# Kernel tuning notes

Hardware: AMD Instinct MI355X
Metric: run time of the kernel (lower is better)

## Reference

```python
import jax, jax.numpy as jnp
import numpy as np

D_MODEL = 1024
N_HEADS = 16
HEAD_DIM = D_MODEL // N_HEADS
LENGTHS = np.array([1536, 1024, 1400, 900, 1200, 1300, 1500, 1000])
OFFSETS = np.concatenate([[0], np.cumsum(LENGTHS)]).astype(np.int32)
N_TOT = int(OFFSETS[-1])
LN_EPS = 1e-5


def _pad_meta(offsets):
    # Static (numpy) gather indices: ragged concat [N,D] -> padded [B,Lmax,D]
    offsets = np.asarray(offsets)
    lengths = np.diff(offsets)
    lmax = int(lengths.max())
    tok = np.arange(lmax)[None, :]                      # [1, Lmax]
    valid = tok < lengths[:, None]                      # [B, Lmax] bool
    src = np.where(valid, offsets[:-1, None] + tok, 0)  # [B, Lmax] int
    return src, valid


def setup_inputs() -> dict:
    key = jax.random.key(0)
    ks = jax.random.split(key, 4)
    s = 1.0 / np.sqrt(D_MODEL)
    return {
        "x": jax.random.normal(ks[0], (N_TOT, D_MODEL), jnp.float32),
        "batch_offsets": jnp.asarray(OFFSETS, jnp.int32),
        "in_proj_w": jax.random.normal(ks[1], (3 * D_MODEL, D_MODEL), jnp.float32) * s,
        "in_proj_b": jnp.zeros((3 * D_MODEL,), jnp.float32),
        "out_w": jax.random.normal(ks[2], (D_MODEL, D_MODEL), jnp.float32) * s,
        "out_b": jnp.zeros((D_MODEL,), jnp.float32),
        "ln_g": jnp.ones((D_MODEL,), jnp.float32),
        "ln_b": jnp.zeros((D_MODEL,), jnp.float32),
    }


def reference(x, batch_offsets, in_proj_w, in_proj_b, out_w, out_b, ln_g, ln_b):
    src, valid = _pad_meta(np.asarray(batch_offsets))
    B, L = valid.shape
    vmask = jnp.asarray(valid)
    # deconcat_add_batch_dim: pad to [B, L, D]
    xp = x[src] * vmask[..., None]
    # pre-LayerNorm
    mu = jnp.mean(xp, axis=-1, keepdims=True)
    var = jnp.mean((xp - mu) ** 2, axis=-1, keepdims=True)
    h = (xp - mu) * jax.lax.rsqrt(var + LN_EPS) * ln_g + ln_b
    # fused qkv projection (torch MHA in_proj)
    qkv = h @ in_proj_w.T + in_proj_b                   # [B, L, 3D]
    q, k, v = jnp.split(qkv, 3, axis=-1)
    def heads(t):
        return t.reshape(B, L, N_HEADS, HEAD_DIM).transpose(0, 2, 1, 3)
    q, k, v = heads(q), heads(k), heads(v)              # [B, H, L, hd]
    scores = jnp.einsum("bhqd,bhkd->bhqk", q, k) / np.sqrt(HEAD_DIM)
    scores = jnp.where(vmask[:, None, None, :], scores, -jnp.inf)
    attn = jax.nn.softmax(scores, axis=-1)
    o = jnp.einsum("bhqk,bhkd->bhqd", attn, v)          # [B, H, L, hd]
    o = o.transpose(0, 2, 1, 3).reshape(B, L, D_MODEL)
    o = o @ out_w.T + out_b
    y = xp + o                                          # residual (dropout p=0)
    # remove_batch_dim_and_concat: unpad back to [N, D]
    return y[vmask]
```

## Files before the change

kernel.cpp:

```cpp
#include <hip/hip_runtime.h>
#include <hip/hip_bf16.h>
#include <stdint.h>

#define D_MODEL 1024
#define QKV_LD  3072
#define N_TOT   9860
#define M_PAD   9984
#define LN_EPS  1e-5f

typedef __bf16 bf16_t;
typedef __bf16 bf16x8 __attribute__((ext_vector_type(8)));
typedef float  f32x4  __attribute__((ext_vector_type(4)));
typedef float  f32x16 __attribute__((ext_vector_type(16)));
typedef uint32_t u32x4 __attribute__((ext_vector_type(4)));

__device__ inline unsigned short f2bf(float f) {
  __bf16 h = (__bf16)f;
  return __builtin_bit_cast(unsigned short, h);
}
__device__ inline int imin(int a, int b) { return a < b ? a : b; }

__device__ inline void plswap(uint32_t& a, uint32_t& b) {
  asm("v_permlane32_swap_b32 %0, %1" : "+v"(a), "+v"(b));
}

__device__ inline void gload_lds16(const bf16_t* g, void* l) {
  __builtin_amdgcn_global_load_lds(
      (const __attribute__((address_space(1))) unsigned int*)g,
      (__attribute__((address_space(3))) unsigned int*)l, 16, 0, 0);
}

__global__ __launch_bounds__(256) void ln_cvt_kernel(const float* __restrict__ x,
                                                     const float* __restrict__ g,
                                                     const float* __restrict__ b,
                                                     bf16_t* __restrict__ hout,
                                                     const float* __restrict__ w_in,
                                                     const float* __restrict__ w_out,
                                                     bf16_t* __restrict__ win,
                                                     bf16_t* __restrict__ wout) {
  int row = blockIdx.x;
  int t = threadIdx.x;
  if (row >= M_PAD) {
    const int n_in = QKV_LD * D_MODEL / 4;
    int i = (row - M_PAD) * 256 + t;
    const float* src;
    ushort4* dst;
    int j;
    if (i < n_in) { src = w_in; dst = (ushort4*)win; j = i; }
    else          { src = w_out; dst = (ushort4*)wout; j = i - n_in; }
    float4 v = ((const float4*)src)[j];
    dst[j] = make_ushort4(f2bf(v.x), f2bf(v.y), f2bf(v.z), f2bf(v.w));
    return;
  }
  if (row >= N_TOT) {
    ((ushort4*)(hout + (size_t)row * D_MODEL))[t] = make_ushort4(0, 0, 0, 0);
    return;
  }
  float4 v = ((const float4*)(x + (size_t)row * D_MODEL))[t];
  float s  = v.x + v.y + v.z + v.w;
  float sq = v.x * v.x + v.y * v.y + v.z * v.z + v.w * v.w;
  #pragma unroll
  for (int off = 1; off < 64; off <<= 1) {
    s  += __shfl_xor(s, off);
    sq += __shfl_xor(sq, off);
  }
  __shared__ float ss[4], ssq[4];
  int wid = t >> 6;
  if ((t & 63) == 0) { ss[wid] = s; ssq[wid] = sq; }
  __syncthreads();
  s  = ss[0] + ss[1] + ss[2] + ss[3];
  sq = ssq[0] + ssq[1] + ssq[2] + ssq[3];
  float mu  = s * (1.0f / 1024.0f);
  float var = sq * (1.0f / 1024.0f) - mu * mu;
  float rs  = rsqrtf(var + LN_EPS);
  float4 gv = ((const float4*)g)[t];
  float4 bv = ((const float4*)b)[t];
  ushort4 o;
  o.x = f2bf((v.x - mu) * rs * gv.x + bv.x);
  o.y = f2bf((v.y - mu) * rs * gv.y + bv.y);
  o.z = f2bf((v.z - mu) * rs * gv.z + bv.z);
  o.w = f2bf((v.w - mu) * rs * gv.w + bv.w);
  ((ushort4*)(hout + (size_t)row * D_MODEL))[t] = o;
}

template<int NCOLS, bool VT>
__global__ __launch_bounds__(512) void gemm256(const bf16_t* __restrict__ A,
                                               const bf16_t* __restrict__ B,
                                               const float* __restrict__ bias,
                                               bf16_t* __restrict__ Cbf,
                                               bf16_t* __restrict__ vt) {
  constexpr int K = 1024, NKT = K / 64;
  constexpr int GX = M_PAD / 256;
  constexpr int NWG = GX * (NCOLS / 256);
  int bid = blockIdx.x;
  {
    constexpr int q = NWG / 8, r = NWG % 8;
    int x = bid & 7, o = bid >> 3;
    bid = (x < r ? x * (q + 1) : r * (q + 1) + (x - r) * q) + o;
  }
  const int tileM = bid % GX;
  const int tileN = bid / GX;
  const int t = threadIdx.x;
  const int lane = t & 63, wid = t >> 6;
  const int wr = wid >> 2, wc = wid & 3;

  __shared__ bf16_t As[2][256 * 64];
  __shared__ bf16_t Bs[2][256 * 64];

  f32x4 acc[8][4];
  #pragma unroll
  for (int m = 0; m < 8; ++m)
    #pragma unroll
    for (int n = 0; n < 4; ++n)
      acc[m][n] = f32x4{0.f, 0.f, 0.f, 0.f};

  const int rowA0 = tileM * 256, rowB0 = tileN * 256;
  const int lrow = lane >> 3;
  const int lch  = lane & 7;

  auto stage = [&](int buf, int kt) {
    const int k0 = kt * 64;
    #pragma unroll
    for (int i = 0; i < 4; ++i) {
      const int r  = wid * 32 + i * 8 + lrow;
      const int sc = lch ^ (r & 7);
      gload_lds16(A + (size_t)(rowA0 + r) * K + k0 + sc * 8,
                  (char*)&As[buf][(wid * 32 + i * 8) * 64]);
      gload_lds16(B + (size_t)(rowB0 + r) * K + k0 + sc * 8,
                  (char*)&Bs[buf][(wid * 32 + i * 8) * 64]);
    }
  };

  stage(0, 0);

  for (int kt = 0; kt < NKT; ++kt) {
    const int cur = kt & 1;
    if (kt + 1 < NKT) {
      stage(cur ^ 1, kt + 1);
      asm volatile("s_waitcnt vmcnt(8)" ::: "memory");
    } else {
      asm volatile("s_waitcnt vmcnt(0)" ::: "memory");
    }
    __builtin_amdgcn_s_barrier();
    __builtin_amdgcn_sched_barrier(0);

    const char* Ab = (const char*)&As[cur][0];
    const char* Bb = (const char*)&Bs[cur][0];

    bf16x8 bfr[4][2];
    #pragma unroll
    for (int n = 0; n < 4; ++n)
      #pragma unroll
      for (int ks = 0; ks < 2; ++ks) {
        int r = wc * 64 + n * 16 + (lane & 15);
        int c = ks * 4 + (lane >> 4);
        bfr[n][ks] = *(const bf16x8*)(Bb + r * 128 + ((c ^ (r & 7)) * 16));
      }
    #pragma unroll
    for (int p = 0; p < 4; ++p) {
      bf16x8 af[2][2];
      #pragma unroll
      for (int mm = 0; mm < 2; ++mm)
        #pragma unroll
        for (int ks = 0; ks < 2; ++ks) {
          int r = wr * 128 + (p * 2 + mm) * 16 + (lane & 15);
          int c = ks * 4 + (lane >> 4);
          af[mm][ks] = *(const bf16x8*)(Ab + r * 128 + ((c ^ (r & 7)) * 16));
        }
      __builtin_amdgcn_s_setprio(1);
      #pragma unroll
      for (int mm = 0; mm < 2; ++mm)
        #pragma unroll
        for (int n = 0; n < 4; ++n)
          #pragma unroll
          for (int ks = 0; ks < 2; ++ks)
            acc[p * 2 + mm][n] =
                __builtin_amdgcn_mfma_f32_16x16x32_bf16(af[mm][ks], bfr[n][ks],
                                                        acc[p * 2 + mm][n], 0, 0, 0);
      __builtin_amdgcn_s_setprio(0);
    }
    __builtin_amdgcn_sched_barrier(0);
    __builtin_amdgcn_s_barrier();
  }

  if (VT && tileN >= 8) {
    static const int OFF_[8] = {0, 1536, 2560, 3960, 4860, 6060, 7360, 8860};
    static const int SH_[8]  = {0, 0, 0, 0, 4, 4, 8, 12};
    #pragma unroll
    for (int m = 0; m < 8; ++m) {
      int rb = tileM * 256 + wr * 128 + m * 16 + ((lane >> 4) << 2);
      if (rb >= N_TOT) continue;
      int bb = 0;
      #pragma unroll
      for (int i = 1; i < 8; ++i) bb += (rb >= OFF_[i]);
      int col0 = rb + SH_[bb];
      #pragma unroll
      for (int n = 0; n < 4; ++n) {
        int cb = tileN * 256 + wc * 64 + n * 16 + (lane & 15);
        float bv = bias[cb];
        float v0 = acc[m][n][0] + bv, v1 = acc[m][n][1] + bv;
        float v2 = acc[m][n][2] + bv, v3 = acc[m][n][3] + bv;
        uint2 u;
        u.x = (uint32_t)f2bf(v0) | ((uint32_t)f2bf(v1) << 16);
        u.y = (uint32_t)f2bf(v2) | ((uint32_t)f2bf(v3) << 16);
        *(uint2*)(vt + (size_t)(cb - 2048) * M_PAD + col0) = u;
      }
    }
  } else {
    #pragma unroll
    for (int m = 0; m < 8; ++m) {
      int rb = tileM * 256 + wr * 128 + m * 16 + ((lane >> 4) << 2);
      #pragma unroll
      for (int n = 0; n < 4; ++n) {
        int cb = tileN * 256 + wc * 64 + n * 16 + (lane & 15);
        float bv = bias[cb];
        #pragma unroll
        for (int j = 0; j < 4; ++j)
          Cbf[(size_t)(rb + j) * NCOLS + cb] = (bf16_t)(acc[m][n][j] + bv);
      }
    }
  }
}

template<int NCOLS, bool FINAL>
__global__ __launch_bounds__(256) void gemm_bt(const bf16_t* __restrict__ A,
                                               const bf16_t* __restrict__ B,
                                               const float* __restrict__ bias,
                                               bf16_t* __restrict__ Cbf,
                                               float* __restrict__ Cf,
                                               const float* __restrict__ resid) {
  constexpr int K = 1024;
  constexpr int GX = M_PAD / 128;
  constexpr int NWG = GX * (NCOLS / 128);
  int bid = blockIdx.x;
  bid = (bid & 7) * (NWG / 8) + (bid >> 3);
  const int tileM = bid % GX;
  const int tileN = bid / GX;
  const int t = threadIdx.x;
  const int lane = t & 63, wid = t >> 6;
  const int wr = wid >> 1, wc = wid & 1;

  __shared__ bf16_t Asm[128 * 64];
  __shared__ bf16_t Bsm[128 * 64];

  f32x4 acc[4][4];
  #pragma unroll
  for (int m = 0; m < 4; ++m)
    #pragma unroll
    for (int n = 0; n < 4; ++n)
      acc[m][n] = f32x4{0.f, 0.f, 0.f, 0.f};

  const int rowA0 = tileM * 128, rowB0 = tileN * 128;
  const int lrow = lane >> 3;
  const int lch  = lane & 7;

  for (int kt = 0; kt < K / 64; ++kt) {
    __syncthreads();
    const int k0 = kt * 64;
    #pragma unroll
    for (int i = 0; i < 4; ++i) {
      const int r  = wid * 32 + i * 8 + lrow;
      const int sc = lch ^ (r & 7);
      gload_lds16(A + (size_t)(rowA0 + r) * K + k0 + sc * 8,
                  (char*)Asm + (wid * 32 + i * 8) * 128);
      gload_lds16(B + (size_t)(rowB0 + r) * K + k0 + sc * 8,
                  (char*)Bsm + (wid * 32 + i * 8) * 128);
    }
    __syncthreads();
    #pragma unroll
    for (int ks = 0; ks < 2; ++ks) {
      bf16x8 af[4], bfr[4];
      #pragma unroll
      for (int m = 0; m < 4; ++m) {
        int r = wr * 64 + m * 16 + (lane & 15);
        int c = ks * 4 + (lane >> 4);
        af[m] = *(const bf16x8*)((const char*)Asm + r * 128 + ((c ^ (r & 7)) * 16));
      }
      #pragma unroll
      for (int n = 0; n < 4; ++n) {
        int r = wc * 64 + n * 16 + (lane & 15);
        int c = ks * 4 + (lane >> 4);
        bfr[n] = *(const bf16x8*)((const char*)Bsm + r * 128 + ((c ^ (r & 7)) * 16));
      }
      #pragma unroll
      for (int m = 0; m < 4; ++m)
        #pragma unroll
        for (int n = 0; n < 4; ++n)
          acc[m][n] = __builtin_amdgcn_mfma_f32_16x16x32_bf16(af[m], bfr[n], acc[m][n], 0, 0, 0);
    }
  }

  #pragma unroll
  for (int m = 0; m < 4; ++m) {
    int rb = tileM * 128 + wr * 64 + m * 16 + ((lane >> 4) << 2);
    #pragma unroll
    for (int n = 0; n < 4; ++n) {
      int cb = tileN * 128 + wc * 64 + n * 16 + (lane & 15);
      float bv = bias[cb];
      #pragma unroll
      for (int j = 0; j < 4; ++j) {
        int grow = rb + j;
        float val = acc[m][n][j] + bv;
        if constexpr (FINAL) {
          if (grow < N_TOT) {
            size_t idx = (size_t)grow * NCOLS + cb;
            Cf[idx] = resid[idx] + val;
          }
        } else {
          Cbf[(size_t)grow * NCOLS + cb] = (bf16_t)val;
        }
      }
    }
  }
}

__global__ __launch_bounds__(256) void attn_mfma(const bf16_t* __restrict__ qkv,
                                                 const bf16_t* __restrict__ vt,
                                                 bf16_t* __restrict__ obuf) {
  static const int off0_[8] = {0, 7360, 2560, 6060, 4860, 1536, 8860, 3960};
  static const int vcol_[8] = {0, 7368, 2560, 6064, 4864, 1536, 8872, 3960};
  static const int len_[8]  = {1536, 1500, 1400, 1300, 1200, 1024, 1000, 900};
  static const int ts_[9]   = {0, 12, 24, 35, 46, 56, 64, 72, 80};
  const int tt = blockIdx.x;
  const int h  = blockIdx.y;
  int b = 0;
  #pragma unroll
  for (int i = 1; i < 8; ++i) b += (tt >= ts_[i]);
  const int L     = len_[b];
  const int kbase = off0_[b];
  const int vcol  = vcol_[b];
  const int q0    = (tt - ts_[b]) * 128;
  const int tok0  = kbase + q0;
  const int nq    = imin(L - q0, 128);

  const int t = threadIdx.x;
  const int lane = t & 63, w = t >> 6;
  const int qcol = lane & 31, hi = lane >> 5;

  __shared__ char Ks[3][8192];
  __shared__ char Vs[3][8192];

  const float MSHIFT = 23.0f;

  const float qs = 0.125f * 1.44269504f;
  bf16x8 qf[4];
  {
    const bf16_t* qp = qkv + (size_t)(tok0 + w * 32 + qcol) * QKV_LD + h * 64;
    #pragma unroll
    for (int c = 0; c < 4; ++c) {
      bf16x8 v = *(const bf16x8*)(qp + c * 16 + hi * 8);
      #pragma unroll
      for (int i = 0; i < 8; ++i) v[i] = (__bf16)((float)v[i] * qs);
      qf[c] = v;
    }
  }

  f32x16 accO[2];
  #pragma unroll
  for (int db = 0; db < 2; ++db)
    #pragma unroll
    for (int i = 0; i < 16; ++i) accO[db][i] = 0.f;
  float lsum = 0.f;

  const int srow = w * 8 + (lane >> 3);
  const int sch  = lane & 7;
  const int sc   = sch ^ (srow & 7);

  auto stage = [&](int buf, int kv0) {
    #pragma unroll
    for (int it = 0; it < 2; ++it) {
      int row = srow + it * 32;
      gload_lds16(qkv + (size_t)(kbase + kv0 + row) * QKV_LD + 1024 + h * 64 + sc * 8,
                  &Ks[buf][w * 1024 + it * 4096]);
      gload_lds16(vt + (size_t)(h * 64 + row) * M_PAD + vcol + kv0 + sc * 8,
                  &Vs[buf][w * 1024 + it * 4096]);
    }
  };

  const int nt = (L + 63) >> 6;
  stage(0, 0);
  stage(1, 64);
  int cur = 0;

  for (int ti = 0; ti < nt; ++ti) {
    const int nk = imin(L - ti * 64, 64);
    if (ti + 1 < nt) {
      asm volatile("s_waitcnt vmcnt(4)" ::: "memory");
    } else {
      asm volatile("s_waitcnt vmcnt(0)" ::: "memory");
    }
    __builtin_amdgcn_s_barrier();
    __builtin_amdgcn_sched_barrier(0);
    if (ti + 2 < nt) {
      int nbuf = cur + 2; if (nbuf >= 3) nbuf -= 3;
      stage(nbuf, (ti + 2) * 64);
    }

    const char* Kb = Ks[cur];
    const char* Vb = Vs[cur];

    f32x16 accS[2];
    #pragma unroll
    for (int kb = 0; kb < 2; ++kb)
      #pragma unroll
      for (int i = 0; i < 16; ++i) accS[kb][i] = 0.f;
    __builtin_amdgcn_s_setprio(1);
    #pragma unroll
    for (int kb = 0; kb < 2; ++kb) {
      int key = kb * 32 + qcol;
      #pragma unroll
      for (int c = 0; c < 4; ++c) {
        bf16x8 kf = *(const bf16x8*)(Kb + key * 128 + (((2 * c + hi) ^ (key & 7)) * 16));
        accS[kb] = __builtin_amdgcn_mfma_f32_32x32x16_bf16(kf, qf[c], accS[kb], 0, 0, 0);
      }
    }
    __builtin_amdgcn_s_setprio(0);

    if (nk < 64) {
      #pragma unroll
      for (int kb = 0; kb < 2; ++kb)
        #pragma unroll
        for (int r = 0; r < 16; ++r)
          if (kb * 32 + (r & 3) + 8 * (r >> 2) + 4 * hi >= nk) accS[kb][r] = -INFINITY;
    }

    bf16x8 pb[2][2];
    #pragma unroll
    for (int kb = 0; kb < 2; ++kb) {
      uint32_t G[4][2];
      #pragma unroll
      for (int j = 0; j < 4; ++j) {
        float p0 = __builtin_amdgcn_exp2f(accS[kb][4 * j + 0] - MSHIFT);
        float p1 = __builtin_amdgcn_exp2f(accS[kb][4 * j + 1] - MSHIFT);
        float p2 = __builtin_amdgcn_exp2f(accS[kb][4 * j + 2] - MSHIFT);
        float p3 = __builtin_amdgcn_exp2f(accS[kb][4 * j + 3] - MSHIFT);
        lsum += (p0 + p1) + (p2 + p3);
        G[j][0] = (uint32_t)f2bf(p0) | ((uint32_t)f2bf(p1) << 16);
        G[j][1] = (uint32_t)f2bf(p2) | ((uint32_t)f2bf(p3) << 16);
      }
      #pragma unroll
      for (int c = 0; c < 2; ++c) {
        uint32_t ax = G[2 * c][0], bx = G[2 * c + 1][0];
        uint32_t ay = G[2 * c][1], by = G[2 * c + 1][1];
        plswap(ax, bx);
        plswap(ay, by);
        u32x4 u; u[0] = ax; u[1] = ay; u[2] = bx; u[3] = by;
        pb[kb][c] = __builtin_bit_cast(bf16x8, u);
      }
    }

    __builtin_amdgcn_s_setprio(1);
    #pragma unroll
    for (int kb = 0; kb < 2; ++kb)
      #pragma unroll
      for (int c = 0; c < 2; ++c) {
        int ch = 4 * kb + 2 * c + hi;
        #pragma unroll
        for (int db = 0; db < 2; ++db) {
          int dim = db * 32 + qcol;
          bf16x8 vf = *(const bf16x8*)(Vb + dim * 128 + ((ch ^ (dim & 7)) * 16));
          accO[db] = __builtin_amdgcn_mfma_f32_32x32x16_bf16(vf, pb[kb][c], accO[db], 0, 0, 0);
        }
      }
    __builtin_amdgcn_s_setprio(0);
    cur = (cur == 2) ? 0 : cur + 1;
  }

  float l = lsum + __shfl_xor(lsum, 32);
  const int qlocal = w * 32 + qcol;
  if (qlocal < nq) {
    float inv = 1.f / l;
    bf16_t* op = obuf + (size_t)(tok0 + qlocal) * D_MODEL + h * 64;
    #pragma unroll
    for (int db = 0; db < 2; ++db)
      #pragma unroll
      for (int rr = 0; rr < 4; ++rr) {
        float v0 = accO[db][4 * rr + 0] * inv;
        float v1 = accO[db][4 * rr + 1] * inv;
        float v2 = accO[db][4 * rr + 2] * inv;
        float v3 = accO[db][4 * rr + 3] * inv;
        uint2 u;
        u.x = (uint32_t)f2bf(v0) | ((uint32_t)f2bf(v1) << 16);
        u.y = (uint32_t)f2bf(v2) | ((uint32_t)f2bf(v3) << 16);
        *(uint2*)(op + db * 32 + rr * 8 + hi * 4) = u;
      }
  }
}

extern "C" void kernel_launch(void* const* d_in, const int* in_sizes, int n_in,
                              void* d_out, int out_size, void* d_ws, size_t ws_size,
                              hipStream_t stream) {
  const float* x     = (const float*)d_in[0];
  const float* w_in  = (const float*)d_in[2];
  const float* b_in  = (const float*)d_in[3];
  const float* w_out = (const float*)d_in[4];
  const float* b_out = (const float*)d_in[5];
  const float* ln_g  = (const float*)d_in[6];
  const float* ln_b  = (const float*)d_in[7];
  float* out = (float*)d_out;

  char* ws = (char*)d_ws;
  const size_t SZ_H   = (size_t)M_PAD * D_MODEL * 2;
  const size_t SZ_QKV = (size_t)M_PAD * QKV_LD * 2;
  const size_t SZ_O   = SZ_H;
  const size_t SZ_WIN = (size_t)QKV_LD * D_MODEL * 2;
  const size_t SZ_WO  = (size_t)D_MODEL * D_MODEL * 2;
  const size_t SZ_VT  = SZ_H;
  if (ws_size < SZ_H + SZ_QKV + SZ_O + SZ_WIN + SZ_WO + SZ_VT) return;

  bf16_t* h_bf    = (bf16_t*)ws;
  bf16_t* qkv_bf  = (bf16_t*)(ws + SZ_H);
  bf16_t* o_bf    = (bf16_t*)(ws + SZ_H + SZ_QKV);
  bf16_t* win_bf  = (bf16_t*)(ws + SZ_H + SZ_QKV + SZ_O);
  bf16_t* wout_bf = (bf16_t*)(ws + SZ_H + SZ_QKV + SZ_O + SZ_WIN);
  bf16_t* vt      = (bf16_t*)(ws + SZ_H + SZ_QKV + SZ_O + SZ_WIN + SZ_WO);

  const int cvt_blocks = (QKV_LD * D_MODEL / 4 + D_MODEL * D_MODEL / 4) / 256;
  ln_cvt_kernel<<<M_PAD + cvt_blocks, 256, 0, stream>>>(
      x, ln_g, ln_b, h_bf, w_in, w_out, win_bf, wout_bf);

  gemm256<QKV_LD, true><<<(M_PAD / 256) * (QKV_LD / 256), 512, 0, stream>>>(
      h_bf, win_bf, b_in, qkv_bf, vt);

  attn_mfma<<<dim3(80, 16), 256, 0, stream>>>(qkv_bf, vt, o_bf);

  gemm_bt<D_MODEL, true><<<(M_PAD / 128) * (D_MODEL / 128), 256, 0, stream>>>(
      o_bf, wout_bf, b_out, nullptr, out, x);
}
```

Baseline: 293.9 us.

## Load K/V fragments directly from global memory instead of LDS triple-buffering

```diff
diff --git a/kernel.cpp b/kernel.cpp
--- a/kernel.cpp
+++ b/kernel.cpp
@@ -337,9 +337,6 @@
   const int lane = t & 63, w = t >> 6;
   const int qcol = lane & 31, hi = lane >> 5;
 
-  __shared__ char Ks[3][8192];
-  __shared__ char Vs[3][8192];
-
   const float MSHIFT = 23.0f;
 
   const float qs = 0.125f * 1.44269504f;
@@ -362,42 +359,23 @@
     for (int i = 0; i < 16; ++i) accO[db][i] = 0.f;
   float lsum = 0.f;
 
-  const int srow = w * 8 + (lane >> 3);
-  const int sch  = lane & 7;
-  const int sc   = sch ^ (srow & 7);
-
-  auto stage = [&](int buf, int kv0) {
-    #pragma unroll
-    for (int it = 0; it < 2; ++it) {
-      int row = srow + it * 32;
-      gload_lds16(qkv + (size_t)(kbase + kv0 + row) * QKV_LD + 1024 + h * 64 + sc * 8,
-                  &Ks[buf][w * 1024 + it * 4096]);
-      gload_lds16(vt + (size_t)(h * 64 + row) * M_PAD + vcol + kv0 + sc * 8,
-                  &Vs[buf][w * 1024 + it * 4096]);
-    }
-  };
+  const bf16_t* Kp = qkv + 1024 + h * 64 + (size_t)0;
+  const bf16_t* Vp = vt + (size_t)(h * 64) * M_PAD + vcol;
 
   const int nt = (L + 63) >> 6;
-  stage(0, 0);
-  stage(1, 64);
-  int cur = 0;
 
   for (int ti = 0; ti < nt; ++ti) {
-    const int nk = imin(L - ti * 64, 64);
-    if (ti + 1 < nt) {
-      asm volatile("s_waitcnt vmcnt(4)" ::: "memory");
-    } else {
-      asm volatile("s_waitcnt vmcnt(0)" ::: "memory");
-    }
-    __builtin_amdgcn_s_barrier();
-    __builtin_amdgcn_sched_barrier(0);
-    if (ti + 2 < nt) {
-      int nbuf = cur + 2; if (nbuf >= 3) nbuf -= 3;
-      stage(nbuf, (ti + 2) * 64);
-    }
-
-    const char* Kb = Ks[cur];
-    const char* Vb = Vs[cur];
+    const int kv0 = ti * 64;
+    const int nk  = imin(L - kv0, 64);
+
+    bf16x8 kf[2][4];
+    #pragma unroll
+    for (int kb = 0; kb < 2; ++kb) {
+      const bf16_t* kp = Kp + (size_t)(kbase + kv0 + kb * 32 + qcol) * QKV_LD + hi * 8;
+      #pragma unroll
+      for (int c = 0; c < 4; ++c)
+        kf[kb][c] = *(const bf16x8*)(kp + c * 16);
+    }
 
     f32x16 accS[2];
     #pragma unroll
@@ -406,15 +384,22 @@
       for (int i = 0; i < 16; ++i) accS[kb][i] = 0.f;
     __builtin_amdgcn_s_setprio(1);
     #pragma unroll
-    for (int kb = 0; kb < 2; ++kb) {
-      int key = kb * 32 + qcol;
-      #pragma unroll
-      for (int c = 0; c < 4; ++c) {
-        bf16x8 kf = *(const bf16x8*)(Kb + key * 128 + (((2 * c + hi) ^ (key & 7)) * 16));
-        accS[kb] = __builtin_amdgcn_mfma_f32_32x32x16_bf16(kf, qf[c], accS[kb], 0, 0, 0);
-      }
-    }
+    for (int kb = 0; kb < 2; ++kb)
+      #pragma unroll
+      for (int c = 0; c < 4; ++c)
+        accS[kb] = __builtin_amdgcn_mfma_f32_32x32x16_bf16(kf[kb][c], qf[c], accS[kb], 0, 0, 0);
     __builtin_amdgcn_s_setprio(0);
+
+    bf16x8 vf[2][2][2];
+    #pragma unroll
+    for (int db = 0; db < 2; ++db) {
+      const bf16_t* vp = Vp + (size_t)(db * 32 + qcol) * M_PAD + kv0;
+      #pragma unroll
+      for (int kb = 0; kb < 2; ++kb)
+        #pragma unroll
+        for (int c = 0; c < 2; ++c)
+          vf[kb][c][db] = *(const bf16x8*)(vp + (4 * kb + 2 * c + hi) * 8);
+    }
 
     if (nk < 64) {
       #pragma unroll
@@ -453,17 +438,11 @@
     #pragma unroll
     for (int kb = 0; kb < 2; ++kb)
       #pragma unroll
-      for (int c = 0; c < 2; ++c) {
-        int ch = 4 * kb + 2 * c + hi;
-        #pragma unroll
-        for (int db = 0; db < 2; ++db) {
-          int dim = db * 32 + qcol;
-          bf16x8 vf = *(const bf16x8*)(Vb + dim * 128 + ((ch ^ (dim & 7)) * 16));
-          accO[db] = __builtin_amdgcn_mfma_f32_32x32x16_bf16(vf, pb[kb][c], accO[db], 0, 0, 0);
-        }
-      }
+      for (int c = 0; c < 2; ++c)
+        #pragma unroll
+        for (int db = 0; db < 2; ++db)
+          accO[db] = __builtin_amdgcn_mfma_f32_32x32x16_bf16(vf[kb][c][db], pb[kb][c], accO[db], 0, 0, 0);
     __builtin_amdgcn_s_setprio(0);
-    cur = (cur == 2) ? 0 : cur + 1;
   }
 
   float l = lsum + __shfl_xor(lsum, 32);
```

Result: slower. 405.0 us (+37.8%).

## Process 256 queries per attention block to reuse staged K/V tiles

Applied to the files above, without the earlier changes.

```diff
diff --git a/kernel.cpp b/kernel.cpp
--- a/kernel.cpp
+++ b/kernel.cpp
@@ -320,7 +320,7 @@
   static const int off0_[8] = {0, 7360, 2560, 6060, 4860, 1536, 8860, 3960};
   static const int vcol_[8] = {0, 7368, 2560, 6064, 4864, 1536, 8872, 3960};
   static const int len_[8]  = {1536, 1500, 1400, 1300, 1200, 1024, 1000, 900};
-  static const int ts_[9]   = {0, 12, 24, 35, 46, 56, 64, 72, 80};
+  static const int ts_[9]   = {0, 6, 12, 18, 24, 29, 33, 37, 41};
   const int tt = blockIdx.x;
   const int h  = blockIdx.y;
   int b = 0;
@@ -329,9 +329,9 @@
   const int L     = len_[b];
   const int kbase = off0_[b];
   const int vcol  = vcol_[b];
-  const int q0    = (tt - ts_[b]) * 128;
+  const int q0    = (tt - ts_[b]) * 256;
   const int tok0  = kbase + q0;
-  const int nq    = imin(L - q0, 128);
+  const int nq    = imin(L - q0, 256);
 
   const int t = threadIdx.x;
   const int lane = t & 63, w = t >> 6;
@@ -343,24 +343,27 @@
   const float MSHIFT = 23.0f;
 
   const float qs = 0.125f * 1.44269504f;
-  bf16x8 qf[4];
-  {
-    const bf16_t* qp = qkv + (size_t)(tok0 + w * 32 + qcol) * QKV_LD + h * 64;
+  bf16x8 qf[2][4];
+  #pragma unroll
+  for (int s = 0; s < 2; ++s) {
+    const bf16_t* qp = qkv + (size_t)(tok0 + s * 128 + w * 32 + qcol) * QKV_LD + h * 64;
     #pragma unroll
     for (int c = 0; c < 4; ++c) {
       bf16x8 v = *(const bf16x8*)(qp + c * 16 + hi * 8);
       #pragma unroll
       for (int i = 0; i < 8; ++i) v[i] = (__bf16)((float)v[i] * qs);
-      qf[c] = v;
-    }
-  }
-
-  f32x16 accO[2];
-  #pragma unroll
-  for (int db = 0; db < 2; ++db)
-    #pragma unroll
-    for (int i = 0; i < 16; ++i) accO[db][i] = 0.f;
-  float lsum = 0.f;
+      qf[s][c] = v;
+    }
+  }
+
+  f32x16 accO[2][2];
+  #pragma unroll
+  for (int s = 0; s < 2; ++s)
+    #pragma unroll
+    for (int db = 0; db < 2; ++db)
+      #pragma unroll
+      for (int i = 0; i < 16; ++i) accO[s][db][i] = 0.f;
+  float lsum0 = 0.f, lsum1 = 0.f;
 
   const int srow = w * 8 + (lane >> 3);
   const int sch  = lane & 7;
@@ -399,11 +402,13 @@
     const char* Kb = Ks[cur];
     const char* Vb = Vs[cur];
 
-    f32x16 accS[2];
-    #pragma unroll
-    for (int kb = 0; kb < 2; ++kb)
-      #pragma unroll
-      for (int i = 0; i < 16; ++i) accS[kb][i] = 0.f;
+    f32x16 accS[2][2];
+    #pragma unroll
+    for (int s = 0; s < 2; ++s)
+      #pragma unroll
+      for (int kb = 0; kb < 2; ++kb)
+        #pragma unroll
+        for (int i = 0; i < 16; ++i) accS[s][kb][i] = 0.f;
     __builtin_amdgcn_s_setprio(1);
     #pragma unroll
     for (int kb = 0; kb < 2; ++kb) {
@@ -411,79 +416,89 @@
       #pragma unroll
       for (int c = 0; c < 4; ++c) {
         bf16x8 kf = *(const bf16x8*)(Kb + key * 128 + (((2 * c + hi) ^ (key & 7)) * 16));
-        accS[kb] = __builtin_amdgcn_mfma_f32_32x32x16_bf16(kf, qf[c], accS[kb], 0, 0, 0);
+        accS[0][kb] = __builtin_amdgcn_mfma_f32_32x32x16_bf16(kf, qf[0][c], accS[0][kb], 0, 0, 0);
+        accS[1][kb] = __builtin_amdgcn_mfma_f32_32x32x16_bf16(kf, qf[1][c], accS[1][kb], 0, 0, 0);
       }
     }
     __builtin_amdgcn_s_setprio(0);
 
     if (nk < 64) {
       #pragma unroll
+      for (int s = 0; s < 2; ++s)
+        #pragma unroll
+        for (int kb = 0; kb < 2; ++kb)
+          #pragma unroll
+          for (int r = 0; r < 16; ++r)
+            if (kb * 32 + (r & 3) + 8 * (r >> 2) + 4 * hi >= nk) accS[s][kb][r] = -INFINITY;
+    }
+
+    #pragma unroll
+    for (int s = 0; s < 2; ++s) {
+      bf16x8 pb[2][2];
+      #pragma unroll
+      for (int kb = 0; kb < 2; ++kb) {
+        uint32_t G[4][2];
+        #pragma unroll
+        for (int j = 0; j < 4; ++j) {
+          float p0 = __builtin_amdgcn_exp2f(accS[s][kb][4 * j + 0] - MSHIFT);
+          float p1 = __builtin_amdgcn_exp2f(accS[s][kb][4 * j + 1] - MSHIFT);
+          float p2 = __builtin_amdgcn_exp2f(accS[s][kb][4 * j + 2] - MSHIFT);
+          float p3 = __builtin_amdgcn_exp2f(accS[s][kb][4 * j + 3] - MSHIFT);
+          if (s == 0) lsum0 += (p0 + p1) + (p2 + p3);
+          else        lsum1 += (p0 + p1) + (p2 + p3);
+          G[j][0] = (uint32_t)f2bf(p0) | ((uint32_t)f2bf(p1) << 16);
+          G[j][1] = (uint32_t)f2bf(p2) | ((uint32_t)f2bf(p3) << 16);
+        }
+        #pragma unroll
+        for (int c = 0; c < 2; ++c) {
+          uint32_t ax = G[2 * c][0], bx = G[2 * c + 1][0];
+          uint32_t ay = G[2 * c][1], by = G[2 * c + 1][1];
+          plswap(ax, bx);
+          plswap(ay, by);
+          u32x4 u; u[0] = ax; u[1] = ay; u[2] = bx; u[3] = by;
+          pb[kb][c] = __builtin_bit_cast(bf16x8, u);
+        }
+      }
+      __builtin_amdgcn_s_setprio(1);
+      #pragma unroll
       for (int kb = 0; kb < 2; ++kb)
         #pragma unroll
-        for (int r = 0; r < 16; ++r)
-          if (kb * 32 + (r & 3) + 8 * (r >> 2) + 4 * hi >= nk) accS[kb][r] = -INFINITY;
-    }
-
-    bf16x8 pb[2][2];
-    #pragma unroll
-    for (int kb = 0; kb < 2; ++kb) {
-      uint32_t G[4][2];
-      #pragma unroll
-      for (int j = 0; j < 4; ++j) {
-        float p0 = __builtin_amdgcn_exp2f(accS[kb][4 * j + 0] - MSHIFT);
-        float p1 = __builtin_amdgcn_exp2f(accS[kb][4 * j + 1] - MSHIFT);
-        float p2 = __builtin_amdgcn_exp2f(accS[kb][4 * j + 2] - MSHIFT);
-        float p3 = __builtin_amdgcn_exp2f(accS[kb][4 * j + 3] - MSHIFT);
-        lsum += (p0 + p1) + (p2 + p3);
-        G[j][0] = (uint32_t)f2bf(p0) | ((uint32_t)f2bf(p1) << 16);
-        G[j][1] = (uint32_t)f2bf(p2) | ((uint32_t)f2bf(p3) << 16);
-      }
-      #pragma unroll
-      for (int c = 0; c < 2; ++c) {
-        uint32_t ax = G[2 * c][0], bx = G[2 * c + 1][0];
-        uint32_t ay = G[2 * c][1], by = G[2 * c + 1][1];
-        plswap(ax, bx);
-        plswap(ay, by);
-        u32x4 u; u[0] = ax; u[1] = ay; u[2] = bx; u[3] = by;
-        pb[kb][c] = __builtin_bit_cast(bf16x8, u);
-      }
-    }
-
-    __builtin_amdgcn_s_setprio(1);
-    #pragma unroll
-    for (int kb = 0; kb < 2; ++kb)
-      #pragma unroll
-      for (int c = 0; c < 2; ++c) {
-        int ch = 4 * kb + 2 * c + hi;
-        #pragma unroll
-        for (int db = 0; db < 2; ++db) {
-          int dim = db * 32 + qcol;
-          bf16x8 vf = *(const bf16x8*)(Vb + dim * 128 + ((ch ^ (dim & 7)) * 16));
-          accO[db] = __builtin_amdgcn_mfma_f32_32x32x16_bf16(vf, pb[kb][c], accO[db], 0, 0, 0);
+        for (int c = 0; c < 2; ++c) {
+          int ch = 4 * kb + 2 * c + hi;
+          #pragma unroll
+          for (int db = 0; db < 2; ++db) {
+            int dim = db * 32 + qcol;
+            bf16x8 vf = *(const bf16x8*)(Vb + dim * 128 + ((ch ^ (dim & 7)) * 16));
+            accO[s][db] = __builtin_amdgcn_mfma_f32_32x32x16_bf16(vf, pb[kb][c], accO[s][db], 0, 0, 0);
+          }
         }
-      }
-    __builtin_amdgcn_s_setprio(0);
+      __builtin_amdgcn_s_setprio(0);
+    }
     cur = (cur == 2) ? 0 : cur + 1;
   }
 
-  float l = lsum + __shfl_xor(lsum, 32);
-  const int qlocal = w * 32 + qcol;
-  if (qlocal < nq) {
-    float inv = 1.f / l;
-    bf16_t* op = obuf + (size_t)(tok0 + qlocal) * D_MODEL + h * 64;
-    #pragma unroll
-    for (int db = 0; db < 2; ++db)
-      #pragma unroll
-      for (int rr = 0; rr < 4; ++rr) {
-        float v0 = accO[db][4 * rr + 0] * inv;
-        float v1 = accO[db][4 * rr + 1] * inv;
-        float v2 = accO[db][4 * rr + 2] * inv;
-        float v3 = accO[db][4 * rr + 3] * inv;
-        uint2 u;
-        u.x = (uint32_t)f2bf(v0) | ((uint32_t)f2bf(v1) << 16);
-        u.y = (uint32_t)f2bf(v2) | ((uint32_t)f2bf(v3) << 16);
-        *(uint2*)(op + db * 32 + rr * 8 + hi * 4) = u;
-      }
+  #pragma unroll
+  for (int s = 0; s < 2; ++s) {
+    float ls = (s == 0) ? lsum0 : lsum1;
+    float l = ls + __shfl_xor(ls, 32);
+    const int qlocal = s * 128 + w * 32 + qcol;
+    if (qlocal < nq) {
+      float inv = 1.f / l;
+      bf16_t* op = obuf + (size_t)(tok0 + qlocal) * D_MODEL + h * 64;
+      #pragma unroll
+      for (int db = 0; db < 2; ++db)
+        #pragma unroll
+        for (int rr = 0; rr < 4; ++rr) {
+          float v0 = accO[s][db][4 * rr + 0] * inv;
+          float v1 = accO[s][db][4 * rr + 1] * inv;
+          float v2 = accO[s][db][4 * rr + 2] * inv;
+          float v3 = accO[s][db][4 * rr + 3] * inv;
+          uint2 u;
+          u.x = (uint32_t)f2bf(v0) | ((uint32_t)f2bf(v1) << 16);
+          u.y = (uint32_t)f2bf(v2) | ((uint32_t)f2bf(v3) << 16);
+          *(uint2*)(op + db * 32 + rr * 8 + hi * 4) = u;
+        }
+    }
   }
 }
 
@@ -522,7 +537,7 @@
   gemm256<QKV_LD, true><<<(M_PAD / 256) * (QKV_LD / 256), 512, 0, stream>>>(
       h_bf, win_bf, b_in, qkv_bf, vt);
 
-  attn_mfma<<<dim3(80, 16), 256, 0, stream>>>(qkv_bf, vt, o_bf);
+  attn_mfma<<<dim3(41, 16), 256, 0, stream>>>(qkv_bf, vt, o_bf);
 
   gemm_bt<D_MODEL, true><<<(M_PAD / 128) * (D_MODEL / 128), 256, 0, stream>>>(
       o_bf, wout_bf, b_out, nullptr, out, x);
```

New measurement: 329.2 us. +12.0%, slower.
